# Performance work log

Measured on AMD Instinct MI355X. Metric: run time of the kernel, lower is better.

Reference implementation:

```python
import jax, jax.numpy as jnp
import numpy as np

N_HEADS = 16
HEAD_DIM = 64
D_MODEL = 1024

def setup_inputs() -> dict:
    key = jax.random.key(0)
    k1, k2, k3 = jax.random.split(key, 3)
    B, S = 4, 2048
    x = jax.random.normal(k1, (B, S, D_MODEL), dtype=jnp.float32)
    Wqkv = jax.random.normal(k2, (D_MODEL, 3 * D_MODEL), dtype=jnp.float32) * (D_MODEL ** -0.5)
    bqkv = jnp.zeros((3 * D_MODEL,), dtype=jnp.float32)
    Wo = jax.random.normal(k3, (D_MODEL, D_MODEL), dtype=jnp.float32) * (D_MODEL ** -0.5)
    bo = jnp.zeros((D_MODEL,), dtype=jnp.float32)
    return {"x": x, "Wqkv": Wqkv, "bqkv": bqkv, "Wo": Wo, "bo": bo}

def reference(x, Wqkv, bqkv, Wo, bo):
    B, S, E = x.shape
    H, D = N_HEADS, HEAD_DIM
    qkv = x @ Wqkv + bqkv                      # [B,S,3E]
    q, k, v = jnp.split(qkv, 3, axis=-1)
    q = q.reshape(B, S, H, D).transpose(0, 2, 1, 3)  # [B,H,S,D]
    k = k.reshape(B, S, H, D).transpose(0, 2, 1, 3)
    v = v.reshape(B, S, H, D).transpose(0, 2, 1, 3)
    scores = jnp.einsum('bhsd,bhtd->bhst', q, k) / jnp.sqrt(jnp.float32(D))
    causal = jnp.tril(jnp.ones((S, S), dtype=bool))
    scores = jnp.where(causal[None, None], scores, jnp.float32(-jnp.inf))
    attn = jax.nn.softmax(scores, axis=-1)
    y = jnp.einsum('bhst,bhtd->bhsd', attn, v)       # [B,H,S,D]
    y = y.transpose(0, 2, 1, 3).reshape(B, S, E)
    return y @ Wo + bo
```

## Files before the change

kernel.cpp:

```cpp
#include <hip/hip_runtime.h>
#include <hip/hip_bf16.h>
#include <stdint.h>

typedef __bf16 bf16;
typedef __bf16 bf16x8 __attribute__((ext_vector_type(8)));
typedef __bf16 bf16x4 __attribute__((ext_vector_type(4)));
typedef float  f32x4  __attribute__((ext_vector_type(4)));
typedef float  f32x16 __attribute__((ext_vector_type(16)));
typedef unsigned u32x2 __attribute__((ext_vector_type(2)));

__device__ __forceinline__ void load_lds16(const void* g, void* l) {
  __builtin_amdgcn_global_load_lds((const __attribute__((address_space(1))) void*)g,
                                   (__attribute__((address_space(3))) void*)l, 16, 0, 0);
}

__device__ __forceinline__ unsigned pk2(float a, float b) {
  union { bf16 h[2]; unsigned u; } t;
  t.h[0] = (bf16)a; t.h[1] = (bf16)b;
  return t.u;
}

#if __has_builtin(__builtin_amdgcn_exp2f)
__device__ __forceinline__ float fexp(float x) { return __builtin_amdgcn_exp2f(x); }
#define QSCALE_F (0.125f * 1.44269504f)
#else
__device__ __forceinline__ float fexp(float x) { return __expf(x); }
#define QSCALE_F 0.125f
#endif

__global__ __launch_bounds__(256) void prep_k(const float* __restrict__ x,
                                              bf16* __restrict__ xb,
                                              const float* __restrict__ wqkv,
                                              bf16* __restrict__ wqt,
                                              const float* __restrict__ wo,
                                              bf16* __restrict__ wot) {
  __shared__ __align__(16) bf16 tile[64 * 72];
  const int bid = blockIdx.x;
  const int t = threadIdx.x;
  if (bid >= 1024) {
    int i = (bid - 1024) * 2048 + t * 8;
    float4 a = *(const float4*)(x + i);
    float4 b = *(const float4*)(x + i + 4);
    bf16x8 o;
    o[0] = (bf16)a.x; o[1] = (bf16)a.y; o[2] = (bf16)a.z; o[3] = (bf16)a.w;
    o[4] = (bf16)b.x; o[5] = (bf16)b.y; o[6] = (bf16)b.z; o[7] = (bf16)b.w;
    *(bf16x8*)(xb + i) = o;
    return;
  }
  const int bx = bid & 63;
  const float* in = (bx < 48) ? wqkv : wo;
  bf16* out = (bx < 48) ? wqt : wot;
  const int N = (bx < 48) ? 3072 : 1024;
  const int n0 = ((bx < 48) ? bx : bx - 48) * 64;
  const int k0 = (bid >> 6) * 64;
  const int K = 1024;
  int r = t >> 2, cq = (t & 3) * 16;
  const float* src = in + (size_t)(k0 + r) * N + n0 + cq;
#pragma unroll
  for (int j = 0; j < 16; j += 4) {
    float4 v = *(const float4*)(src + j);
    tile[r * 72 + cq + j + 0] = (bf16)v.x;
    tile[r * 72 + cq + j + 1] = (bf16)v.y;
    tile[r * 72 + cq + j + 2] = (bf16)v.z;
    tile[r * 72 + cq + j + 3] = (bf16)v.w;
  }
  __syncthreads();
  bf16x8 r0, r1;
#pragma unroll
  for (int j = 0; j < 8; ++j) r0[j] = tile[(cq + j) * 72 + r];
#pragma unroll
  for (int j = 0; j < 8; ++j) r1[j] = tile[(cq + 8 + j) * 72 + r];
  bf16* dst = out + (size_t)(n0 + r) * K + k0 + cq;
  *(bf16x8*)(dst) = r0;
  *(bf16x8*)(dst + 8) = r1;
}

template <int EPI>
__global__ __launch_bounds__(256) void gemm_bt(const bf16* __restrict__ A,
                                               const bf16* __restrict__ BT,
                                               const float* __restrict__ bias,
                                               float* __restrict__ Cf,
                                               bf16* __restrict__ qk,
                                               bf16* __restrict__ vt,
                                               int M, int N, int K) {
  __shared__ __align__(16) bf16 As[128 * 64];
  __shared__ __align__(16) bf16 Bs[128 * 64];
  const int tid = threadIdx.x;
  const int w = tid >> 6, l = tid & 63;
  const int g = l >> 4, c = l & 15;
  const int wm = w >> 1, wn = w & 1;

  const int lin = blockIdx.y * gridDim.x + blockIdx.x;
  const int q = (gridDim.x * gridDim.y) >> 3;
  const int swz = (lin & 7) * q + (lin >> 3);
  const int brow = (swz / gridDim.x) * 128;
  const int bcol = (swz % gridDim.x) * 128;

  int alane[4];
#pragma unroll
  for (int i = 0; i < 4; ++i) {
    int row = w * 32 + i * 8 + (l >> 3);
    alane[i] = row * K + (((l & 7) ^ (row & 7)) * 8);
  }

  f32x4 acc[4][4];
#pragma unroll
  for (int m = 0; m < 4; ++m)
#pragma unroll
    for (int n = 0; n < 4; ++n) acc[m][n] = f32x4{0.f, 0.f, 0.f, 0.f};

  const bf16* Abase = A + (size_t)brow * K;
  const bf16* Bbase = BT + (size_t)bcol * K;
  const int nkt = K >> 6;
  for (int kt = 0; kt < nkt; ++kt) {
    if (kt) __syncthreads();
    const bf16* Akt = Abase + kt * 64;
    const bf16* Bkt = Bbase + kt * 64;
#pragma unroll
    for (int i = 0; i < 4; ++i) {
      load_lds16(Akt + alane[i], &As[(w * 32 + i * 8) * 64]);
      load_lds16(Bkt + alane[i], &Bs[(w * 32 + i * 8) * 64]);
    }
    asm volatile("s_waitcnt vmcnt(0)" ::: "memory");
    __syncthreads();

#pragma unroll
    for (int ks = 0; ks < 2; ++ks) {
      bf16x8 af[4], bfr[4];
#pragma unroll
      for (int m = 0; m < 4; ++m)
        af[m] = *(const bf16x8*)&As[(wm * 64 + m * 16 + c) * 64 + (((ks * 4 + g) ^ (c & 7)) * 8)];
#pragma unroll
      for (int n = 0; n < 4; ++n)
        bfr[n] = *(const bf16x8*)&Bs[(wn * 64 + n * 16 + c) * 64 + (((ks * 4 + g) ^ (c & 7)) * 8)];
#pragma unroll
      for (int m = 0; m < 4; ++m)
#pragma unroll
        for (int n = 0; n < 4; ++n)
          acc[m][n] = __builtin_amdgcn_mfma_f32_16x16x32_bf16(af[m], bfr[n], acc[m][n], 0, 0, 0);
    }
  }

#pragma unroll
  for (int m = 0; m < 4; ++m) {
    int row_l = wm * 64 + m * 16 + (l >> 4) * 4;
#pragma unroll
    for (int n = 0; n < 4; ++n) {
      int col = bcol + wn * 64 + n * 16 + c;
      float bv = bias[col];
      if (EPI == 0) {
        if (bcol < 2048) {
#pragma unroll
          for (int r = 0; r < 4; ++r) {
            int row = brow + row_l + r;
            qk[(size_t)row * 2048 + col] = (bf16)(acc[m][n][r] + bv);
          }
        } else {
          int hh = (col - 2048) >> 6, dd = (col - 2048) & 63;
          int row0 = brow + row_l;
          int bb = row0 >> 11, ss = row0 & 2047;
          bf16x4 pk;
#pragma unroll
          for (int r = 0; r < 4; ++r) pk[r] = (bf16)(acc[m][n][r] + bv);
          *(bf16x4*)&vt[((size_t)(bb * 16 + hh) * 64 + dd) * 2048 + ss] = pk;
        }
      } else {
#pragma unroll
        for (int r = 0; r < 4; ++r) {
          int row = brow + row_l + r;
          Cf[(size_t)row * N + col] = acc[m][n][r] + bv;
        }
      }
    }
  }
}

__global__ __launch_bounds__(128) void attn_k(const bf16* __restrict__ qkbuf,
                                              const bf16* __restrict__ vtbuf,
                                              bf16* __restrict__ aout) {
  __shared__ __align__(16) bf16 Ks[2][64 * 64];
  __shared__ __align__(16) bf16 Vs[2][64 * 64];

  const int tid = threadIdx.x;
  const int w = tid >> 6, l = tid & 63;
  const int c32 = l & 31, hi = l >> 5;

  const int bid = blockIdx.x;
  const int xcd = bid & 7;
  const int idx = bid >> 3;
  const int bh = xcd * 8 + (idx >> 4);
  const int j = idx & 15;
  const int p = j >> 1, h0 = j & 1;
  const int b = bh >> 4, h = bh & 15;

  const bf16* ksrc = qkbuf + (size_t)(b * 2048) * 2048 + 1024 + h * 64;
  const bf16* vsrc = vtbuf + (size_t)(bh * 64) * 2048;

  int lane4[4];
#pragma unroll
  for (int i = 0; i < 4; ++i) {
    int rr = w * 32 + i * 8 + (l >> 3);
    lane4[i] = rr * 2048 + (((l & 7) ^ (rr & 7)) * 8);
  }

#pragma unroll 1
  for (int item = 0; item < 2; ++item) {
    const int qblk = item == 0 ? 15 - p : p;
    const int half = item == 0 ? h0 : 1 - h0;
    const int nt = 2 * qblk + half + 1;
    const int qw = qblk * 128 + half * 64 + w * 32;
    const int myq = qw + c32;

    const size_t qoff = (size_t)(b * 2048 + myq) * 2048 + h * 64;
    bf16x8 qf[4];
#pragma unroll
    for (int t = 0; t < 4; ++t) {
      bf16x8 vq = *(const bf16x8*)&qkbuf[qoff + t * 16 + hi * 8];
#pragma unroll
      for (int jj = 0; jj < 8; ++jj) vq[jj] = (bf16)((float)vq[jj] * QSCALE_F);
      qf[t] = vq;
    }

    float l_r = 0.f;
    f32x16 o[2];
    o[0] = (f32x16)(0.f); o[1] = (f32x16)(0.f);

#define STAGE_TILE(buf, KV0)                                                        \
    {                                                                               \
      const bf16* kt_k = ksrc + (size_t)(KV0) * 2048;                               \
      const bf16* kt_v = vsrc + (KV0);                                              \
      _Pragma("unroll")                                                             \
      for (int i = 0; i < 4; ++i) {                                                 \
        load_lds16(kt_k + lane4[i], &Ks[buf][(w * 32 + i * 8) * 64]);               \
        load_lds16(kt_v + lane4[i], &Vs[buf][(w * 32 + i * 8) * 64]);               \
      }                                                                             \
    }

    STAGE_TILE(0, 0)
    asm volatile("s_waitcnt vmcnt(0)" ::: "memory");
    __syncthreads();

    int cur = 0;
    for (int kt = 0; kt < nt; ++kt) {
      const int kv0 = kt * 64;
      if (kt + 1 < nt) STAGE_TILE(cur ^ 1, kv0 + 64)

      const bf16* kb = &Ks[cur][0];
      const bf16* vb = &Vs[cur][0];

      f32x16 st[2];
      st[0] = (f32x16)(0.f); st[1] = (f32x16)(0.f);
      __builtin_amdgcn_s_setprio(1);
#pragma unroll
      for (int t = 0; t < 4; ++t) {
#pragma unroll
        for (int ks = 0; ks < 2; ++ks) {
          int kv = ks * 32 + c32;
          bf16x8 kf = *(const bf16x8*)&kb[kv * 64 + (((2 * t + hi) ^ (kv & 7)) * 8)];
          st[ks] = __builtin_amdgcn_mfma_f32_32x32x16_bf16(kf, qf[t], st[ks], 0, 0, 0);
        }
      }
      __builtin_amdgcn_s_setprio(0);

      if (kv0 + 63 > qw) {
#pragma unroll
        for (int ks = 0; ks < 2; ++ks)
#pragma unroll
          for (int r = 0; r < 16; ++r) {
            int kvidx = kv0 + ks * 32 + (r & 3) + 8 * (r >> 2) + 4 * hi;
            if (kvidx > myq) st[ks][r] = -1e30f;
          }
      }

      float s0 = 0.f, s1 = 0.f, s2 = 0.f, s3 = 0.f;
#pragma unroll
      for (int ks = 0; ks < 2; ++ks)
#pragma unroll
        for (int r = 0; r < 16; r += 4) {
          float p0 = fexp(st[ks][r + 0]);
          float p1 = fexp(st[ks][r + 1]);
          float p2 = fexp(st[ks][r + 2]);
          float p3 = fexp(st[ks][r + 3]);
          st[ks][r + 0] = p0; st[ks][r + 1] = p1;
          st[ks][r + 2] = p2; st[ks][r + 3] = p3;
          s0 += p0; s1 += p1; s2 += p2; s3 += p3;
        }
      l_r += (s0 + s1) + (s2 + s3);

      bf16x8 pfr[4];
#pragma unroll
      for (int t = 0; t < 4; ++t) {
        const int ks = t >> 1, eb = (t & 1) * 8;
        unsigned w0 = pk2(st[ks][eb + 0], st[ks][eb + 1]);
        unsigned w1 = pk2(st[ks][eb + 2], st[ks][eb + 3]);
        unsigned w2 = pk2(st[ks][eb + 4], st[ks][eb + 5]);
        unsigned w3 = pk2(st[ks][eb + 6], st[ks][eb + 7]);
        u32x2 r02 = __builtin_amdgcn_permlane32_swap(w0, w2, false, false);
        u32x2 r13 = __builtin_amdgcn_permlane32_swap(w1, w3, false, false);
        union { unsigned u[4]; bf16x8 v; } pf;
        pf.u[0] = r02[0]; pf.u[1] = r13[0]; pf.u[2] = r02[1]; pf.u[3] = r13[1];
        pfr[t] = pf.v;
      }

      __builtin_amdgcn_s_setprio(1);
#pragma unroll
      for (int t = 0; t < 4; ++t) {
#pragma unroll
        for (int ds = 0; ds < 2; ++ds) {
          int d = ds * 32 + c32;
          bf16x8 vf = *(const bf16x8*)&vb[d * 64 + (((2 * t + hi) ^ (d & 7)) * 8)];
          o[ds] = __builtin_amdgcn_mfma_f32_32x32x16_bf16(vf, pfr[t], o[ds], 0, 0, 0);
        }
      }
      __builtin_amdgcn_s_setprio(0);

      asm volatile("s_waitcnt vmcnt(0)" ::: "memory");
      __syncthreads();
      cur ^= 1;
    }

    u32x2 lres = __builtin_amdgcn_permlane32_swap(__float_as_uint(l_r),
                                                  __float_as_uint(l_r), false, false);
    const float inv = 1.0f / (__uint_as_float(lres[0]) + __uint_as_float(lres[1]));
    bf16* orow = aout + (size_t)(b * 2048 + myq) * 1024 + h * 64;
#pragma unroll
    for (int ds = 0; ds < 2; ++ds)
#pragma unroll
      for (int rg = 0; rg < 4; ++rg) {
        bf16x4 pk;
#pragma unroll
        for (int i = 0; i < 4; ++i) pk[i] = (bf16)(o[ds][rg * 4 + i] * inv);
        *(bf16x4*)&orow[ds * 32 + rg * 8 + hi * 4] = pk;
      }
#undef STAGE_TILE
  }
}

extern "C" void kernel_launch(void* const* d_in, const int* in_sizes, int n_in,
                              void* d_out, int out_size, void* d_ws, size_t ws_size,
                              hipStream_t stream) {
  const float* x    = (const float*)d_in[0];
  const float* Wqkv = (const float*)d_in[1];
  const float* bqkv = (const float*)d_in[2];
  const float* Wo   = (const float*)d_in[3];
  const float* bo   = (const float*)d_in[4];
  float* out = (float*)d_out;

  char* ws = (char*)d_ws;
  bf16* xb   = (bf16*)(ws);
  bf16* wqt  = (bf16*)(ws + 16777216);
  bf16* wot  = (bf16*)(ws + 23068672);
  bf16* qkb  = (bf16*)(ws + 25165824);
  bf16* vtb  = (bf16*)(ws + 58720256);
  bf16* aob  = (bf16*)(ws + 75497472);

  prep_k<<<dim3(5120), dim3(256), 0, stream>>>(x, xb, Wqkv, wqt, Wo, wot);
  gemm_bt<0><<<dim3(24, 64), dim3(256), 0, stream>>>(xb, wqt, bqkv, nullptr, qkb, vtb,
                                                     8192, 3072, 1024);
  attn_k<<<dim3(1024), dim3(128), 0, stream>>>(qkb, vtb, aob);
  gemm_bt<1><<<dim3(8, 64), dim3(256), 0, stream>>>(aob, wot, bo, out, nullptr, nullptr,
                                                    8192, 1024, 1024);
}
```

Before: 170.7 us.

## Software-pipeline attention loop: overlap next QK MFMA with current softmax/PV

Restructures the attention inner loop so the QK^T MFMAs for tile t+1 are issued before the softmax and PV work for tile t, using two ping-pong score register sets. K is staged two tiles ahead and V one tile ahead, with the loop unrolled by two to keep buffer indices static. The aim is to interleave exp/pack VALU work with matrix-core work and hide load latency. The cost is higher register pressure from the extra score accumulators and more complex prologue and epilogue handling.

```diff
diff --git a/kernel.cpp b/kernel.cpp
--- a/kernel.cpp
+++ b/kernel.cpp
@@ -203,6 +203,90 @@
     lane4[i] = rr * 2048 + (((l & 7) ^ (rr & 7)) * 8);
   }
 
+#define STAGE_K(T, DST)                                                             \
+    { const bf16* _s = ksrc + (size_t)(T) * (64 * 2048);                            \
+      _Pragma("unroll")                                                             \
+      for (int i = 0; i < 4; ++i)                                                   \
+        load_lds16(_s + lane4[i], (DST) + (w * 32 + i * 8) * 64); }
+#define STAGE_V(T, DST)                                                             \
+    { const bf16* _s = vsrc + (T) * 64;                                             \
+      _Pragma("unroll")                                                             \
+      for (int i = 0; i < 4; ++i)                                                   \
+        load_lds16(_s + lane4[i], (DST) + (w * 32 + i * 8) * 64); }
+
+#define QK_TILE(PDST, KB)                                                           \
+    { PDST[0] = (f32x16)(0.f); PDST[1] = (f32x16)(0.f);                             \
+      __builtin_amdgcn_s_setprio(1);                                                \
+      _Pragma("unroll")                                                             \
+      for (int t = 0; t < 4; ++t) {                                                 \
+        _Pragma("unroll")                                                           \
+        for (int ks = 0; ks < 2; ++ks) {                                            \
+          int kv = ks * 32 + c32;                                                   \
+          bf16x8 kf = *(const bf16x8*)&(KB)[kv * 64 + (((2 * t + hi) ^ (kv & 7)) * 8)]; \
+          PDST[ks] = __builtin_amdgcn_mfma_f32_32x32x16_bf16(kf, qf[t], PDST[ks], 0, 0, 0); \
+        }                                                                           \
+      }                                                                             \
+      __builtin_amdgcn_s_setprio(0); }
+
+#define SM_PV(PSRC, TT, VB)                                                         \
+    { const int kv0_ = (TT) * 64;                                                   \
+      if (kv0_ + 63 > qw) {                                                         \
+        _Pragma("unroll")                                                           \
+        for (int ks = 0; ks < 2; ++ks)                                              \
+          _Pragma("unroll")                                                         \
+          for (int r = 0; r < 16; ++r) {                                            \
+            int kvidx = kv0_ + ks * 32 + (r & 3) + 8 * (r >> 2) + 4 * hi;           \
+            if (kvidx > myq) PSRC[ks][r] = -1e30f;                                  \
+          }                                                                         \
+      }                                                                             \
+      float s0 = 0.f, s1 = 0.f, s2 = 0.f, s3 = 0.f;                                 \
+      _Pragma("unroll")                                                             \
+      for (int ks = 0; ks < 2; ++ks)                                                \
+        _Pragma("unroll")                                                           \
+        for (int r = 0; r < 16; r += 4) {                                           \
+          float p0 = fexp(PSRC[ks][r + 0]);                                         \
+          float p1 = fexp(PSRC[ks][r + 1]);                                         \
+          float p2 = fexp(PSRC[ks][r + 2]);                                         \
+          float p3 = fexp(PSRC[ks][r + 3]);                                         \
+          PSRC[ks][r + 0] = p0; PSRC[ks][r + 1] = p1;                               \
+          PSRC[ks][r + 2] = p2; PSRC[ks][r + 3] = p3;                               \
+          s0 += p0; s1 += p1; s2 += p2; s3 += p3;                                   \
+        }                                                                           \
+      l_r += (s0 + s1) + (s2 + s3);                                                 \
+      bf16x8 pfr[4];                                                                \
+      _Pragma("unroll")                                                             \
+      for (int t = 0; t < 4; ++t) {                                                 \
+        const int ks = t >> 1, eb = (t & 1) * 8;                                    \
+        unsigned w0 = pk2(PSRC[ks][eb + 0], PSRC[ks][eb + 1]);                      \
+        unsigned w1 = pk2(PSRC[ks][eb + 2], PSRC[ks][eb + 3]);                      \
+        unsigned w2 = pk2(PSRC[ks][eb + 4], PSRC[ks][eb + 5]);                      \
+        unsigned w3 = pk2(PSRC[ks][eb + 6], PSRC[ks][eb + 7]);                      \
+        u32x2 r02 = __builtin_amdgcn_permlane32_swap(w0, w2, false, false);         \
+        u32x2 r13 = __builtin_amdgcn_permlane32_swap(w1, w3, false, false);         \
+        union { unsigned u[4]; bf16x8 v; } pf;                                      \
+        pf.u[0] = r02[0]; pf.u[1] = r13[0]; pf.u[2] = r02[1]; pf.u[3] = r13[1];     \
+        pfr[t] = pf.v;                                                              \
+      }                                                                             \
+      __builtin_amdgcn_s_setprio(1);                                                \
+      _Pragma("unroll")                                                             \
+      for (int t = 0; t < 4; ++t) {                                                 \
+        _Pragma("unroll")                                                           \
+        for (int ds = 0; ds < 2; ++ds) {                                            \
+          int d = ds * 32 + c32;                                                    \
+          bf16x8 vf = *(const bf16x8*)&(VB)[d * 64 + (((2 * t + hi) ^ (d & 7)) * 8)]; \
+          o[ds] = __builtin_amdgcn_mfma_f32_32x32x16_bf16(vf, pfr[t], o[ds], 0, 0, 0); \
+        }                                                                           \
+      }                                                                             \
+      __builtin_amdgcn_s_setprio(0); }
+
+#define AITER(PA, PB, TT, KSG, KRD, VSG, VRD)                                       \
+    { STAGE_K((TT) + 2, KSG)                                                        \
+      STAGE_V((TT) + 1, VSG)                                                        \
+      QK_TILE(PB, KRD)                                                              \
+      SM_PV(PA, TT, VRD)                                                            \
+      asm volatile("s_waitcnt vmcnt(0)" ::: "memory");                              \
+      __syncthreads(); }
+
 #pragma unroll 1
   for (int item = 0; item < 2; ++item) {
     const int qblk = item == 0 ? 15 - p : p;
@@ -224,100 +308,29 @@
     float l_r = 0.f;
     f32x16 o[2];
     o[0] = (f32x16)(0.f); o[1] = (f32x16)(0.f);
-
-#define STAGE_TILE(buf, KV0)                                                        \
-    {                                                                               \
-      const bf16* kt_k = ksrc + (size_t)(KV0) * 2048;                               \
-      const bf16* kt_v = vsrc + (KV0);                                              \
-      _Pragma("unroll")                                                             \
-      for (int i = 0; i < 4; ++i) {                                                 \
-        load_lds16(kt_k + lane4[i], &Ks[buf][(w * 32 + i * 8) * 64]);               \
-        load_lds16(kt_v + lane4[i], &Vs[buf][(w * 32 + i * 8) * 64]);               \
-      }                                                                             \
-    }
-
-    STAGE_TILE(0, 0)
+    f32x16 stA[2], stB[2];
+
+    STAGE_K(0, &Ks[0][0])
+    STAGE_V(0, &Vs[0][0])
     asm volatile("s_waitcnt vmcnt(0)" ::: "memory");
     __syncthreads();
-
-    int cur = 0;
-    for (int kt = 0; kt < nt; ++kt) {
-      const int kv0 = kt * 64;
-      if (kt + 1 < nt) STAGE_TILE(cur ^ 1, kv0 + 64)
-
-      const bf16* kb = &Ks[cur][0];
-      const bf16* vb = &Vs[cur][0];
-
-      f32x16 st[2];
-      st[0] = (f32x16)(0.f); st[1] = (f32x16)(0.f);
-      __builtin_amdgcn_s_setprio(1);
-#pragma unroll
-      for (int t = 0; t < 4; ++t) {
-#pragma unroll
-        for (int ks = 0; ks < 2; ++ks) {
-          int kv = ks * 32 + c32;
-          bf16x8 kf = *(const bf16x8*)&kb[kv * 64 + (((2 * t + hi) ^ (kv & 7)) * 8)];
-          st[ks] = __builtin_amdgcn_mfma_f32_32x32x16_bf16(kf, qf[t], st[ks], 0, 0, 0);
-        }
-      }
-      __builtin_amdgcn_s_setprio(0);
-
-      if (kv0 + 63 > qw) {
-#pragma unroll
-        for (int ks = 0; ks < 2; ++ks)
-#pragma unroll
-          for (int r = 0; r < 16; ++r) {
-            int kvidx = kv0 + ks * 32 + (r & 3) + 8 * (r >> 2) + 4 * hi;
-            if (kvidx > myq) st[ks][r] = -1e30f;
-          }
-      }
-
-      float s0 = 0.f, s1 = 0.f, s2 = 0.f, s3 = 0.f;
-#pragma unroll
-      for (int ks = 0; ks < 2; ++ks)
-#pragma unroll
-        for (int r = 0; r < 16; r += 4) {
-          float p0 = fexp(st[ks][r + 0]);
-          float p1 = fexp(st[ks][r + 1]);
-          float p2 = fexp(st[ks][r + 2]);
-          float p3 = fexp(st[ks][r + 3]);
-          st[ks][r + 0] = p0; st[ks][r + 1] = p1;
-          st[ks][r + 2] = p2; st[ks][r + 3] = p3;
-          s0 += p0; s1 += p1; s2 += p2; s3 += p3;
-        }
-      l_r += (s0 + s1) + (s2 + s3);
-
-      bf16x8 pfr[4];
-#pragma unroll
-      for (int t = 0; t < 4; ++t) {
-        const int ks = t >> 1, eb = (t & 1) * 8;
-        unsigned w0 = pk2(st[ks][eb + 0], st[ks][eb + 1]);
-        unsigned w1 = pk2(st[ks][eb + 2], st[ks][eb + 3]);
-        unsigned w2 = pk2(st[ks][eb + 4], st[ks][eb + 5]);
-        unsigned w3 = pk2(st[ks][eb + 6], st[ks][eb + 7]);
-        u32x2 r02 = __builtin_amdgcn_permlane32_swap(w0, w2, false, false);
-        u32x2 r13 = __builtin_amdgcn_permlane32_swap(w1, w3, false, false);
-        union { unsigned u[4]; bf16x8 v; } pf;
-        pf.u[0] = r02[0]; pf.u[1] = r13[0]; pf.u[2] = r02[1]; pf.u[3] = r13[1];
-        pfr[t] = pf.v;
-      }
-
-      __builtin_amdgcn_s_setprio(1);
-#pragma unroll
-      for (int t = 0; t < 4; ++t) {
-#pragma unroll
-        for (int ds = 0; ds < 2; ++ds) {
-          int d = ds * 32 + c32;
-          bf16x8 vf = *(const bf16x8*)&vb[d * 64 + (((2 * t + hi) ^ (d & 7)) * 8)];
-          o[ds] = __builtin_amdgcn_mfma_f32_32x32x16_bf16(vf, pfr[t], o[ds], 0, 0, 0);
-        }
-      }
-      __builtin_amdgcn_s_setprio(0);
-
-      asm volatile("s_waitcnt vmcnt(0)" ::: "memory");
-      __syncthreads();
-      cur ^= 1;
-    }
+    QK_TILE(stA, &Ks[0][0])
+    STAGE_K(1, &Ks[1][0])
+    asm volatile("s_waitcnt vmcnt(0)" ::: "memory");
+    __syncthreads();
+
+    int kt = 0;
+    for (; kt + 2 < nt; kt += 2) {
+      AITER(stA, stB, kt,     &Ks[0][0], &Ks[1][0], &Vs[1][0], &Vs[0][0])
+      AITER(stB, stA, kt + 1, &Ks[1][0], &Ks[0][0], &Vs[0][0], &Vs[1][0])
+    }
+    if (kt + 1 < nt) {
+      AITER(stA, stB, kt, &Ks[0][0], &Ks[1][0], &Vs[1][0], &Vs[0][0])
+      SM_PV(stB, kt + 1, &Vs[1][0])
+    } else {
+      SM_PV(stA, kt, &Vs[0][0])
+    }
+    __syncthreads();
 
     u32x2 lres = __builtin_amdgcn_permlane32_swap(__float_as_uint(l_r),
                                                   __float_as_uint(l_r), false, false);
@@ -332,8 +345,12 @@
         for (int i = 0; i < 4; ++i) pk[i] = (bf16)(o[ds][rg * 4 + i] * inv);
         *(bf16x4*)&orow[ds * 32 + rg * 8 + hi * 4] = pk;
       }
-#undef STAGE_TILE
-  }
+  }
+#undef AITER
+#undef SM_PV
+#undef QK_TILE
+#undef STAGE_V
+#undef STAGE_K
 }
 
 extern "C" void kernel_launch(void* const* d_in, const int* in_sizes, int n_in,
```

After: 180.6 us. 5.8% more time.
